# Kernel tuning notes

Measured on AMD Instinct MI355X. Metric: run time of the kernel, lower is better.

Reference implementation:

```python
import jax, jax.numpy as jnp
import numpy as np

N_NODES = 100000
N_EDGES = 1600000
N_FEAT = 128
HIDDEN = 128
EMB = 256
N_GROUPS = 16
N_GRAPHS = 512


def gcn_conv(x, edge_index, W, b, num_nodes):
    # PyG GCNConv: x' = D^{-1/2} (A + I) D^{-1/2} (x W) + b
    h = x @ W                                   # [N, out]
    loop = jnp.arange(num_nodes, dtype=edge_index.dtype)
    src = jnp.concatenate([edge_index[0], loop])
    dst = jnp.concatenate([edge_index[1], loop])
    ones = jnp.ones(src.shape[0], dtype=h.dtype)
    deg = jax.ops.segment_sum(ones, dst, num_segments=num_nodes)  # >=1 due to self loops
    dinv = jax.lax.rsqrt(deg)
    norm = dinv[src] * dinv[dst]                # [E+N]
    msg = h[src] * norm[:, None]                # gather + scale
    out = jax.ops.segment_sum(msg, dst, num_segments=num_nodes)   # scatter-add
    return out + b


def global_mean_pool(x, batch, num_graphs):
    s = jax.ops.segment_sum(x, batch, num_segments=num_graphs)
    cnt = jax.ops.segment_sum(jnp.ones(x.shape[0], dtype=x.dtype), batch, num_segments=num_graphs)
    return s / jnp.maximum(cnt, 1.0)[:, None]


def setup_inputs() -> dict:
    key = jax.random.key(0)
    ks = jax.random.split(key, 10)
    x = jax.random.normal(ks[0], (N_NODES, N_FEAT), dtype=jnp.float32)
    edge_index = jax.random.randint(ks[1], (2, N_EDGES), 0, N_NODES, dtype=jnp.int64 if jax.config.jax_enable_x64 else jnp.int32)
    batch = jnp.sort(jax.random.randint(ks[2], (N_NODES,), 0, N_GRAPHS))
    def glorot(k, shape):
        lim = np.sqrt(6.0 / (shape[0] + shape[1]))
        return jax.random.uniform(k, shape, jnp.float32, -lim, lim)
    W1 = glorot(ks[3], (N_FEAT, HIDDEN)); b1 = jnp.zeros((HIDDEN,), jnp.float32)
    W2 = glorot(ks[4], (HIDDEN, EMB));    b2 = jnp.zeros((EMB,), jnp.float32)
    Wg = glorot(ks[5], (EMB, N_GROUPS));  bg = jnp.zeros((N_GROUPS,), jnp.float32)
    return {"x": x, "edge_index": edge_index, "batch": batch, "num_graphs": N_GRAPHS,
            "W1": W1, "b1": b1, "W2": W2, "b2": b2, "Wg": Wg, "bg": bg}


def reference(x, edge_index, batch, num_graphs, W1, b1, W2, b2, Wg, bg):
    n = x.shape[0]
    h = jax.nn.relu(gcn_conv(x, edge_index, W1, b1, n))
    # dropout(p=0.5) is identity in eval mode
    h = gcn_conv(h, edge_index, W2, b2, n)
    emb = global_mean_pool(h, batch, num_graphs)      # [G, EMB]
    group_logits = emb @ Wg + bg                      # [G, N_GROUPS]
    return (emb, group_logits)
```

## Files before the change

### kernel.cpp

```cpp
#include <hip/hip_runtime.h>
#include <hip/hip_fp16.h>


#define TPB 256
#define CHUNK 4096
#define MAXB 512
#define SUBS 8
#define SRCMASK 0x1FFFF

typedef _Float16 half8 __attribute__((ext_vector_type(8)));
typedef float floatx4 __attribute__((ext_vector_type(4)));

__device__ __forceinline__ void exscan512(int* a, int* part, int t) {
    int x0 = a[2 * t], x1 = a[2 * t + 1];
    part[t] = x0 + x1;
    __syncthreads();
    for (int off = 1; off < 256; off <<= 1) {
        int v = (t >= off) ? part[t - off] : 0;
        __syncthreads();
        part[t] += v;
        __syncthreads();
    }
    int base = (t > 0) ? part[t - 1] : 0;
    a[2 * t] = base;
    a[2 * t + 1] = base + x0;
    __syncthreads();
}

__global__ __launch_bounds__(256) void k1_bucket(const int* __restrict__ ei, int E,
                                                 int B, int nchunks,
                                                 unsigned* __restrict__ sorted,
                                                 int* __restrict__ histT,
                                                 int* __restrict__ sstartT,
                                                 int* __restrict__ bucketTot) {
    __shared__ int hcnt[MAXB], hoff[MAXB], hcur[MAXB], part[256];
    int c = blockIdx.x, t = threadIdx.x;
    int e0 = c * CHUNK;
    int m = E - e0; if (m > CHUNK) m = CHUNK;
    for (int i = t; i < MAXB; i += 256) { hcnt[i] = 0; hcur[i] = 0; }
    __syncthreads();
    for (int i = t; i < m; i += 256)
        atomicAdd(&hcnt[ei[E + e0 + i] >> 8], 1);
    __syncthreads();
    for (int i = t; i < MAXB; i += 256) hoff[i] = hcnt[i];
    __syncthreads();
    exscan512(hoff, part, t);
    for (int i = t; i < B; i += 256) {
        histT[(size_t)c * B + i]   = hcnt[i];
        sstartT[(size_t)c * B + i] = e0 + hoff[i];
        if (hcnt[i] > 0) atomicAdd(&bucketTot[i], hcnt[i]);
    }
    __syncthreads();
    for (int i = t; i < m; i += 256) {
        int src = ei[e0 + i], dst = ei[E + e0 + i];
        int b = dst >> 8;
        int pos = e0 + hoff[b] + atomicAdd(&hcur[b], 1);
        sorted[pos] = (unsigned)src | ((unsigned)(dst & 255) << 17);
    }
}

#define SLICE_SETUP                                                             \
    int b = blockIdx.x, sub = blockIdx.y, t = threadIdx.x;                      \
    int cpg = (nchunks + SUBS - 1) / SUBS;                                      \
    int c0 = sub * cpg;                                                         \
    int c1 = c0 + cpg; if (c1 > nchunks) c1 = nchunks;                          \
    int nc = c1 - c0; if (nc < 0) nc = 0;                                       \
    if (t < nc) {                                                               \
        slen[t]   = histT[(size_t)(c0 + t) * B + b];                            \
        sstart[t] = sstartT[(size_t)(c0 + t) * B + b];                          \
    }                                                                           \
    __syncthreads();                                                            \
    if (t == 0) {                                                               \
        int run = 0;                                                            \
        for (int i2 = 0; i2 < nc; ++i2) { soff[i2] = run; run += slen[i2]; }    \
        soff[nc] = run;                                                         \
    }                                                                           \
    __syncthreads();                                                            \
    int T = soff[nc];

#define SLICE_EDGE(i)                                                           \
    int lo = 0, hi = nc - 1;                                                    \
    while (lo < hi) { int mid = (lo + hi + 1) >> 1;                             \
                      if (soff[mid] <= (i)) lo = mid; else hi = mid - 1; }      \
    unsigned w = sorted[sstart[lo] + ((i) - soff[lo])];

__global__ __launch_bounds__(256) void k3a_deg(const unsigned* __restrict__ sorted,
                                               const int* __restrict__ histT,
                                               const int* __restrict__ sstartT,
                                               int* __restrict__ deg,
                                               int n, int B, int nchunks) {
    __shared__ int slen[64], sstart[64], soff[65];
    __shared__ int ncnt[256];
    SLICE_SETUP
    ncnt[t] = 0;
    __syncthreads();
    for (int i = t; i < T; i += 256) {
        SLICE_EDGE(i)
        atomicAdd(&ncnt[(w >> 17) & 255], 1);
    }
    __syncthreads();
    int v = (b << 8) + t;
    if (v < n && ncnt[t] > 0) atomicAdd(&deg[v], ncnt[t]);
}

__global__ __launch_bounds__(256) void k3b_offs(const int* __restrict__ deg,
                                                const int* __restrict__ bucketTot,
                                                const int* __restrict__ batch,
                                                int* __restrict__ offs,
                                                float* __restrict__ dinv,
                                                int* __restrict__ cnt, int n) {
    __shared__ int a[512], part[256];
    __shared__ int baseS;
    int b = blockIdx.x, t = threadIdx.x;
    int s = 0;
    for (int i = t; i < b; i += 256) s += bucketTot[i];
    part[t] = s;
    __syncthreads();
    for (int off = 128; off > 0; off >>= 1) {
        if (t < off) part[t] += part[t + off];
        __syncthreads();
    }
    if (t == 0) baseS = part[0];
    __syncthreads();
    int base = baseS;
    int v = (b << 8) + t;
    int dg = (v < n) ? deg[v] : 0;
    a[t] = dg; a[t + 256] = 0;
    __syncthreads();
    exscan512(a, part, t);
    if (v < n) {
        offs[v] = base + a[t];
        dinv[v] = rsqrtf((float)(dg + 1));
        atomicAdd(&cnt[batch[v]], 1);
    }
}

__global__ __launch_bounds__(256) void k3c_scatter(const unsigned* __restrict__ sorted,
                                                   const int* __restrict__ histT,
                                                   const int* __restrict__ sstartT,
                                                   const int* __restrict__ offs,
                                                   int* __restrict__ cursor,
                                                   int* __restrict__ adj,
                                                   int B, int nchunks) {
    __shared__ int slen[64], sstart[64], soff[65];
    SLICE_SETUP
    int vb = b << 8;
    for (int i = t; i < T; i += 256) {
        SLICE_EDGE(i)
        int dst = vb + (int)((w >> 17) & 255);
        int pos = offs[dst] + atomicAdd(&cursor[dst], 1);
        adj[pos] = (int)(w & SRCMASK);
    }
}

__global__ void prep_wt(const float* __restrict__ W, __half* __restrict__ Wt) {
    int t = blockIdx.x * blockDim.x + threadIdx.x;
    int c = t & 127, k = t >> 7;
    Wt[c * 128 + k] = __float2half(W[(size_t)k * 128 + c]);
}

__global__ __launch_bounds__(256) void gemm1_mfma(const float* __restrict__ X,
                                                  const __half* __restrict__ Wt,
                                                  const float* __restrict__ dinv,
                                                  __half* __restrict__ out, int n) {
    __shared__ __align__(16) unsigned char As[64 * 128 * 2];
    __shared__ __align__(16) unsigned char Bs[128 * 128 * 2];
    int t = threadIdx.x;
    int wid = t >> 6, lane = t & 63;
    int qw = lane >> 4, lr = lane & 15;
    int rowBase = blockIdx.x * 64;

#pragma unroll
    for (int c = 0; c < 4; ++c) {
        int id = c * 256 + t;
        int r = id >> 4, kc = id & 15;
        int gr = rowBase + r;
        float4 x0, x1;
        if (gr < n) {
            const float4* src = (const float4*)(X + (size_t)gr * 128 + kc * 8);
            x0 = src[0]; x1 = src[1];
        } else {
            x0 = make_float4(0.f, 0.f, 0.f, 0.f); x1 = x0;
        }
        __half2 h0 = __floats2half2_rn(x0.x, x0.y);
        __half2 h1 = __floats2half2_rn(x0.z, x0.w);
        __half2 h2 = __floats2half2_rn(x1.x, x1.y);
        __half2 h3 = __floats2half2_rn(x1.z, x1.w);
        uint4 w;
        w.x = *(unsigned int*)&h0; w.y = *(unsigned int*)&h1;
        w.z = *(unsigned int*)&h2; w.w = *(unsigned int*)&h3;
        int byte = (r * 256 + kc * 16) ^ ((r & 7) << 4);
        *(uint4*)(As + byte) = w;
    }
#pragma unroll
    for (int c = 0; c < 8; ++c) {
        int id = c * 256 + t;
        int cr = id >> 4, kc = id & 15;
        uint4 w = *(const uint4*)(Wt + (size_t)cr * 128 + kc * 8);
        int byte = (cr * 256 + kc * 16) ^ ((cr & 7) << 4);
        *(uint4*)(Bs + byte) = w;
    }
    __syncthreads();

    floatx4 acc[4][2] = {};
#pragma unroll
    for (int ks = 0; ks < 4; ++ks) {
        int kb = ks * 32 + qw * 8;
        half8 a[4], b[2];
#pragma unroll
        for (int m = 0; m < 4; ++m) {
            int row = m * 16 + lr;
            int byte = (row * 256 + kb * 2) ^ ((row & 7) << 4);
            a[m] = *(const half8*)(As + byte);
        }
#pragma unroll
        for (int nn = 0; nn < 2; ++nn) {
            int col = wid * 32 + nn * 16 + lr;
            int byte = (col * 256 + kb * 2) ^ ((col & 7) << 4);
            b[nn] = *(const half8*)(Bs + byte);
        }
#pragma unroll
        for (int m = 0; m < 4; ++m)
#pragma unroll
            for (int nn = 0; nn < 2; ++nn)
                acc[m][nn] = __builtin_amdgcn_mfma_f32_16x16x32_f16(a[m], b[nn], acc[m][nn], 0, 0, 0);
    }

#pragma unroll
    for (int m = 0; m < 4; ++m) {
#pragma unroll
        for (int q = 0; q < 4; ++q) {
            int gr = rowBase + m * 16 + qw * 4 + q;
            if (gr < n) {
                float dv = dinv[gr];
#pragma unroll
                for (int nn = 0; nn < 2; ++nn) {
                    int col = wid * 32 + nn * 16 + lr;
                    out[(size_t)gr * 128 + col] = __float2half(acc[m][nn][q] * dv);
                }
            }
        }
    }
}

__device__ __forceinline__ void acc_h2(unsigned int rv, float2& a) {
    float2 f = __half22float2(*(__half2*)&rv);
    a.x += f.x; a.y += f.y;
}
#define ROWP(buf, u) ((const unsigned int*)((buf) + (size_t)(u) * 128))

#define PIPE_GATHER(buf)                                                        \
    int nb = d >> 3;                                                            \
    int i = nb << 3;                                                            \
    if (nb > 0) {                                                               \
        int u0 = adj[start+0], u1 = adj[start+1], u2 = adj[start+2],            \
            u3 = adj[start+3], u4 = adj[start+4], u5 = adj[start+5],            \
            u6 = adj[start+6], u7 = adj[start+7];                               \
        unsigned c0 = ROWP(buf,u0)[lane], c1 = ROWP(buf,u1)[lane];              \
        unsigned c2 = ROWP(buf,u2)[lane], c3 = ROWP(buf,u3)[lane];              \
        unsigned c4 = ROWP(buf,u4)[lane], c5 = ROWP(buf,u5)[lane];              \
        unsigned c6 = ROWP(buf,u6)[lane], c7 = ROWP(buf,u7)[lane];              \
        for (int bq = 1; bq < nb; ++bq) {                                       \
            int bs = start + (bq << 3);                                         \
            int t0 = adj[bs+0], t1 = adj[bs+1], t2 = adj[bs+2], t3 = adj[bs+3]; \
            int t4 = adj[bs+4], t5 = adj[bs+5], t6 = adj[bs+6], t7 = adj[bs+7]; \
            unsigned n0 = ROWP(buf,t0)[lane], n1 = ROWP(buf,t1)[lane];          \
            unsigned n2 = ROWP(buf,t2)[lane], n3 = ROWP(buf,t3)[lane];          \
            unsigned n4 = ROWP(buf,t4)[lane], n5 = ROWP(buf,t5)[lane];          \
            unsigned n6 = ROWP(buf,t6)[lane], n7 = ROWP(buf,t7)[lane];          \
            acc_h2(c0, a0); acc_h2(c1, a1); acc_h2(c2, a2); acc_h2(c3, a3);     \
            acc_h2(c4, a0); acc_h2(c5, a1); acc_h2(c6, a2); acc_h2(c7, a3);     \
            c0 = n0; c1 = n1; c2 = n2; c3 = n3;                                 \
            c4 = n4; c5 = n5; c6 = n6; c7 = n7;                                 \
        }                                                                       \
        acc_h2(c0, a0); acc_h2(c1, a1); acc_h2(c2, a2); acc_h2(c3, a3);         \
        acc_h2(c4, a0); acc_h2(c5, a1); acc_h2(c6, a2); acc_h2(c7, a3);         \
    }                                                                           \
    for (; i + 3 < d; i += 4) {                                                 \
        int u0 = adj[start+i+0], u1 = adj[start+i+1];                           \
        int u2 = adj[start+i+2], u3 = adj[start+i+3];                           \
        unsigned r0 = ROWP(buf,u0)[lane], r1 = ROWP(buf,u1)[lane];              \
        unsigned r2 = ROWP(buf,u2)[lane], r3 = ROWP(buf,u3)[lane];              \
        acc_h2(r0, a0); acc_h2(r1, a1); acc_h2(r2, a2); acc_h2(r3, a3);         \
    }                                                                           \
    for (; i < d; ++i) acc_h2(ROWP(buf, adj[start + i])[lane], a0);

__global__ void gather1(const __half* __restrict__ hs, const int* __restrict__ adj,
                        const int* __restrict__ offs, const int* __restrict__ deg,
                        const float* __restrict__ dinv, const float* __restrict__ b1,
                        __half* __restrict__ gs, int n) {
    int wave = threadIdx.x >> 6;
    int lane = threadIdx.x & 63;
    int v = blockIdx.x * 4 + wave;
    if (v >= n) return;
    float2 a0 = make_float2(0.f, 0.f), a1 = a0, a2 = a0, a3 = a0;
    acc_h2(ROWP(hs, v)[lane], a0);
    int start = __builtin_amdgcn_readfirstlane(offs[v]);
    int d     = __builtin_amdgcn_readfirstlane(deg[v]);
    PIPE_GATHER(hs)
    float accx = (a0.x + a1.x) + (a2.x + a3.x);
    float accy = (a0.y + a1.y) + (a2.y + a3.y);
    float dv = dinv[v];
    float2 bb = ((const float2*)b1)[lane];
    float g0 = fmaxf(accx * dv + bb.x, 0.f) * dv;
    float g1 = fmaxf(accy * dv + bb.y, 0.f) * dv;
    __half2 h = __floats2half2_rn(g0, g1);
    ((unsigned int*)(gs + (size_t)v * 128))[lane] = *(unsigned int*)&h;
}

__global__ void gather2_pool(const __half* __restrict__ gs, const int* __restrict__ adj,
                             const int* __restrict__ offs, const int* __restrict__ deg,
                             const float* __restrict__ dinv, const int* __restrict__ batch,
                             float* __restrict__ poolsum, int n) {
    __shared__ float poolacc[128];
    int t = threadIdx.x;
    int wave = t >> 6;
    int lane = t & 63;
    if (t < 128) poolacc[t] = 0.f;
    int gref = batch[blockIdx.x * 4];
    __syncthreads();
    int v = blockIdx.x * 4 + wave;
    if (v < n) {
        float2 a0 = make_float2(0.f, 0.f), a1 = a0, a2 = a0, a3 = a0;
        acc_h2(ROWP(gs, v)[lane], a0);
        int start = __builtin_amdgcn_readfirstlane(offs[v]);
        int d     = __builtin_amdgcn_readfirstlane(deg[v]);
        PIPE_GATHER(gs)
        float accx = (a0.x + a1.x) + (a2.x + a3.x);
        float accy = (a0.y + a1.y) + (a2.y + a3.y);
        float dv = dinv[v];
        int g = batch[v];
        if (g == gref) {
            atomicAdd(&poolacc[lane * 2 + 0], accx * dv);
            atomicAdd(&poolacc[lane * 2 + 1], accy * dv);
        } else {
            float* p = poolsum + (size_t)g * 128;
            atomicAdd(&p[lane * 2 + 0], accx * dv);
            atomicAdd(&p[lane * 2 + 1], accy * dv);
        }
    }
    __syncthreads();
    if (t < 128) {
        float s = poolacc[t];
        if (s != 0.f) atomicAdd(&poolsum[(size_t)gref * 128 + t], s);
    }
}

__global__ void head(const float* __restrict__ poolsum, const int* __restrict__ cnt,
                     const float* __restrict__ W2, const float* __restrict__ b2,
                     const float* __restrict__ Wg, const float* __restrict__ bg,
                     float* __restrict__ out, int G) {
    __shared__ float pm[128];
    __shared__ float emb[256];
    int g = blockIdx.x, t = threadIdx.x;
    float inv = 1.f / fmaxf((float)cnt[g], 1.f);
    if (t < 128) pm[t] = poolsum[(size_t)g * 128 + t] * inv;
    __syncthreads();
    float acc = b2[t];
    for (int k = 0; k < 128; ++k) acc += pm[k] * W2[k * 256 + t];
    out[(size_t)g * 256 + t] = acc;
    emb[t] = acc;
    __syncthreads();
    if (t < 16) {
        float a = bg[t];
        for (int j = 0; j < 256; ++j) a += emb[j] * Wg[j * 16 + t];
        out[(size_t)G * 256 + g * 16 + t] = a;
    }
}

extern "C" void kernel_launch(void* const* d_in, const int* in_sizes, int n_in,
                              void* d_out, int out_size, void* d_ws, size_t ws_size,
                              hipStream_t stream) {
    const float* x     = (const float*)d_in[0];
    const int*   ei    = (const int*)d_in[1];
    const int*   batch = (const int*)d_in[2];
    const float* W1    = (const float*)d_in[4];
    const float* b1    = (const float*)d_in[5];
    const float* W2    = (const float*)d_in[6];
    const float* b2    = (const float*)d_in[7];
    const float* Wg    = (const float*)d_in[8];
    const float* bg    = (const float*)d_in[9];
    float* out = (float*)d_out;

    int n = in_sizes[0] / 128;
    int E = in_sizes[1] / 2;
    int G = out_size / (256 + 16);
    int B = (n + 255) >> 8;
    int nchunks = (E + CHUNK - 1) / CHUNK;

    char* ws = (char*)d_ws;
    auto alloc = [&](size_t bytes) {
        char* p = ws;
        ws += (bytes + 255) & ~(size_t)255;
        return p;
    };
    char*   zbase     = ws;
    int*    deg       = (int*)alloc((size_t)n * 4);
    int*    cursor    = (int*)alloc((size_t)n * 4);
    int*    bucketTot = (int*)alloc((size_t)(B + 1) * 4);
    int*    cnt       = (int*)alloc((size_t)G * 4);
    float*  poolsum   = (float*)alloc((size_t)G * 128 * 4);
    size_t  zbytes    = (size_t)(ws - zbase);
    float*    dinv    = (float*)alloc((size_t)n * 4);
    int*      offs    = (int*)alloc((size_t)n * 4);
    int*      adj     = (int*)alloc((size_t)E * 4);
    unsigned* sorted  = (unsigned*)alloc((size_t)E * 4);
    int*      histT   = (int*)alloc((size_t)B * nchunks * 4);
    int*      sstartT = (int*)alloc((size_t)B * nchunks * 4);
    __half*   Wt      = (__half*)alloc(128 * 128 * 2);
    __half*   hs1     = (__half*)alloc((size_t)n * 128 * 2);
    __half*   gs1     = (__half*)alloc((size_t)n * 128 * 2);

    hipMemsetAsync(zbase, 0, zbytes, stream);

    k1_bucket<<<nchunks, 256, 0, stream>>>(ei, E, B, nchunks, sorted, histT, sstartT,
                                           bucketTot);
    k3a_deg<<<dim3(B, SUBS), 256, 0, stream>>>(sorted, histT, sstartT, deg, n, B, nchunks);
    k3b_offs<<<B, 256, 0, stream>>>(deg, bucketTot, batch, offs, dinv, cnt, n);
    k3c_scatter<<<dim3(B, SUBS), 256, 0, stream>>>(sorted, histT, sstartT, offs, cursor,
                                                   adj, B, nchunks);

    prep_wt<<<64, TPB, 0, stream>>>(W1, Wt);
    gemm1_mfma<<<(n + 63) / 64, 256, 0, stream>>>(x, Wt, dinv, hs1, n);
    gather1<<<(n + 3) / 4, 256, 0, stream>>>(hs1, adj, offs, deg, dinv, b1, gs1, n);
    gather2_pool<<<(n + 3) / 4, 256, 0, stream>>>(gs1, adj, offs, deg, dinv, batch, poolsum, n);
    head<<<G, 256, 0, stream>>>(poolsum, cnt, W2, b2, Wg, bg, out, G);
}
```

Measured before the change: 361.3 us.

## Replace global degree and cursor atomics with per-subslice counts and LDS cursors

The degree kernel now writes one count per (subslice, node) instead of doing global atomics into deg. The offset kernel sums the subslice counts, scans them, and writes a starting offset back for each subslice. The scatter kernel then loads these offsets into shared memory and uses LDS atomics instead of global atomics on a cursor array. This drops the global atomic traffic and the zeroing of deg and cursor, at the cost of an extra SUBS×n int buffer that is read and written.

```diff
diff --git a/kernel.cpp b/kernel.cpp
--- a/kernel.cpp
+++ b/kernel.cpp
@@ -87,8 +87,8 @@
 __global__ __launch_bounds__(256) void k3a_deg(const unsigned* __restrict__ sorted,
                                                const int* __restrict__ histT,
                                                const int* __restrict__ sstartT,
-                                               int* __restrict__ deg,
-                                               int n, int B, int nchunks) {
+                                               int* __restrict__ degSub,
+                                               int B, int nchunks) {
     __shared__ int slen[64], sstart[64], soff[65];
     __shared__ int ncnt[256];
     SLICE_SETUP
@@ -99,16 +99,16 @@
         atomicAdd(&ncnt[(w >> 17) & 255], 1);
     }
     __syncthreads();
-    int v = (b << 8) + t;
-    if (v < n && ncnt[t] > 0) atomicAdd(&deg[v], ncnt[t]);
-}
-
-__global__ __launch_bounds__(256) void k3b_offs(const int* __restrict__ deg,
+    degSub[(size_t)sub * (B << 8) + (b << 8) + t] = ncnt[t];
+}
+
+__global__ __launch_bounds__(256) void k3b_offs(int* __restrict__ degSub,
                                                 const int* __restrict__ bucketTot,
                                                 const int* __restrict__ batch,
                                                 int* __restrict__ offs,
+                                                int* __restrict__ deg,
                                                 float* __restrict__ dinv,
-                                                int* __restrict__ cnt, int n) {
+                                                int* __restrict__ cnt, int n, int B) {
     __shared__ int a[512], part[256];
     __shared__ int baseS;
     int b = blockIdx.x, t = threadIdx.x;
@@ -123,13 +123,23 @@
     if (t == 0) baseS = part[0];
     __syncthreads();
     int base = baseS;
+    size_t stride = (size_t)(B << 8);
+    size_t vi = (size_t)(b << 8) + t;
+    int ds[SUBS];
+    int dg = 0;
+#pragma unroll
+    for (int q = 0; q < SUBS; ++q) { ds[q] = degSub[q * stride + vi]; dg += ds[q]; }
+    a[t] = dg; a[t + 256] = 0;
+    __syncthreads();
+    exscan512(a, part, t);
     int v = (b << 8) + t;
-    int dg = (v < n) ? deg[v] : 0;
-    a[t] = dg; a[t + 256] = 0;
-    __syncthreads();
-    exscan512(a, part, t);
+    int vbase = base + a[t];
+    int run = vbase;
+#pragma unroll
+    for (int q = 0; q < SUBS; ++q) { int c = ds[q]; degSub[q * stride + vi] = run; run += c; }
     if (v < n) {
-        offs[v] = base + a[t];
+        offs[v] = vbase;
+        deg[v]  = dg;
         dinv[v] = rsqrtf((float)(dg + 1));
         atomicAdd(&cnt[batch[v]], 1);
     }
@@ -138,17 +148,18 @@
 __global__ __launch_bounds__(256) void k3c_scatter(const unsigned* __restrict__ sorted,
                                                    const int* __restrict__ histT,
                                                    const int* __restrict__ sstartT,
-                                                   const int* __restrict__ offs,
-                                                   int* __restrict__ cursor,
+                                                   const int* __restrict__ degSub,
                                                    int* __restrict__ adj,
                                                    int B, int nchunks) {
     __shared__ int slen[64], sstart[64], soff[65];
+    __shared__ int cur[256];
     SLICE_SETUP
-    int vb = b << 8;
+    cur[t] = degSub[(size_t)sub * (B << 8) + (b << 8) + t];
+    __syncthreads();
     for (int i = t; i < T; i += 256) {
         SLICE_EDGE(i)
-        int dst = vb + (int)((w >> 17) & 255);
-        int pos = offs[dst] + atomicAdd(&cursor[dst], 1);
+        int r = (w >> 17) & 255;
+        int pos = atomicAdd(&cur[r], 1);
         adj[pos] = (int)(w & SRCMASK);
     }
 }
@@ -395,14 +406,14 @@
         return p;
     };
     char*   zbase     = ws;
-    int*    deg       = (int*)alloc((size_t)n * 4);
-    int*    cursor    = (int*)alloc((size_t)n * 4);
     int*    bucketTot = (int*)alloc((size_t)(B + 1) * 4);
     int*    cnt       = (int*)alloc((size_t)G * 4);
     float*  poolsum   = (float*)alloc((size_t)G * 128 * 4);
     size_t  zbytes    = (size_t)(ws - zbase);
+    int*      deg     = (int*)alloc((size_t)n * 4);
     float*    dinv    = (float*)alloc((size_t)n * 4);
     int*      offs    = (int*)alloc((size_t)n * 4);
+    int*      degSub  = (int*)alloc((size_t)SUBS * ((size_t)B << 8) * 4);
     int*      adj     = (int*)alloc((size_t)E * 4);
     unsigned* sorted  = (unsigned*)alloc((size_t)E * 4);
     int*      histT   = (int*)alloc((size_t)B * nchunks * 4);
@@ -415,9 +426,9 @@
 
     k1_bucket<<<nchunks, 256, 0, stream>>>(ei, E, B, nchunks, sorted, histT, sstartT,
                                            bucketTot);
-    k3a_deg<<<dim3(B, SUBS), 256, 0, stream>>>(sorted, histT, sstartT, deg, n, B, nchunks);
-    k3b_offs<<<B, 256, 0, stream>>>(deg, bucketTot, batch, offs, dinv, cnt, n);
-    k3c_scatter<<<dim3(B, SUBS), 256, 0, stream>>>(sorted, histT, sstartT, offs, cursor,
+    k3a_deg<<<dim3(B, SUBS), 256, 0, stream>>>(sorted, histT, sstartT, degSub, B, nchunks);
+    k3b_offs<<<B, 256, 0, stream>>>(degSub, bucketTot, batch, offs, deg, dinv, cnt, n, B);
+    k3c_scatter<<<dim3(B, SUBS), 256, 0, stream>>>(sorted, histT, sstartT, degSub,
                                                    adj, B, nchunks);
 
     prep_wt<<<64, TPB, 0, stream>>>(W1, Wt);
```

Measured after the change: 340.4 us. -5.8%, faster.
